# Kernel tuning notes

Hardware: AMD Instinct MI355X
Metric: run time of the kernel (lower is better)

## Reference

```python
import jax, jax.numpy as jnp
import numpy as np

# lower-triangular (row, col) positions in the packed order used by the torch loop:
# index order is (j,i) for j in 0..2, i in 0..j -> (0,0),(1,0),(1,1),(2,0),(2,1),(2,2)
_ROWS = jnp.array([0, 1, 1, 2, 2, 2])
_COLS = jnp.array([0, 0, 1, 0, 1, 2])


def setup_inputs() -> dict:
    key = jax.random.key(0)
    bn, seq_len = 4096, 1024
    chol_cov = jax.random.normal(key, (bn, seq_len, 6), dtype=jnp.float32)
    return {"chol_cov": chol_cov}


def reference(chol_cov) -> jnp.ndarray:
    bn, seq_len, _ = chol_cov.shape
    # scatter packed values into lower-triangular 3x3 L: [bn, seq, 3, 3]
    L = jnp.zeros((bn, seq_len, 3, 3), dtype=chol_cov.dtype)
    L = L.at[..., _ROWS, _COLS].set(chol_cov)
    # Q = L @ L^T, batched tiny 3x3 matmul -> symmetric covariance
    Q = jnp.einsum('bsij,bskj->bsik', L, L)
    return Q
```

## Files before the change

### kernel.cpp

```cpp
#include <hip/hip_runtime.h>


#define THREADS 256
#define ITEMS_PER_BLOCK 1024

__global__ __launch_bounds__(THREADS) void chol_to_cov_kernel(
    const float* __restrict__ in, float* __restrict__ out, long long n_items) {
  __shared__ float s_in[ITEMS_PER_BLOCK * 6];
  __shared__ float s_out[ITEMS_PER_BLOCK * 9];

  const int tid = threadIdx.x;
  const long long block_base = (long long)blockIdx.x * ITEMS_PER_BLOCK;

  if (block_base + ITEMS_PER_BLOCK <= n_items) {
    const float4* __restrict__ in4 = (const float4*)(in + block_base * 6);
    float4* s_in4 = (float4*)s_in;
#pragma unroll
    for (int k = 0; k < 6; k++) {
      s_in4[tid + k * THREADS] = in4[tid + k * THREADS];
    }
    __syncthreads();

#pragma unroll
    for (int k = 0; k < 4; k++) {
      const int item = tid + k * THREADS;
      const float* s = s_in + item * 6;
      const float a = s[0], b = s[1], c = s[2], d = s[3], e = s[4], f = s[5];
      const float q00 = a * a;
      const float q01 = a * b;
      const float q02 = a * d;
      const float q11 = b * b + c * c;
      const float q12 = b * d + c * e;
      const float q22 = d * d + e * e + f * f;
      float* o = s_out + item * 9;
      o[0] = q00;
      o[1] = q01;
      o[2] = q02;
      o[3] = q01;
      o[4] = q11;
      o[5] = q12;
      o[6] = q02;
      o[7] = q12;
      o[8] = q22;
    }
    __syncthreads();

    float4* __restrict__ out4 = (float4*)(out + block_base * 9);
    const float4* s_out4 = (const float4*)s_out;
#pragma unroll
    for (int k = 0; k < 9; k++) {
      out4[tid + k * THREADS] = s_out4[tid + k * THREADS];
    }
  } else {
    for (long long it = block_base + tid; it < n_items; it += THREADS) {
      const float a = in[it * 6 + 0];
      const float b = in[it * 6 + 1];
      const float c = in[it * 6 + 2];
      const float d = in[it * 6 + 3];
      const float e = in[it * 6 + 4];
      const float f = in[it * 6 + 5];
      float* o = out + it * 9;
      o[0] = a * a;
      o[1] = a * b;
      o[2] = a * d;
      o[3] = a * b;
      o[4] = b * b + c * c;
      o[5] = b * d + c * e;
      o[6] = a * d;
      o[7] = b * d + c * e;
      o[8] = d * d + e * e + f * f;
    }
  }
}

extern "C" void kernel_launch(void* const* d_in, const int* in_sizes, int n_in,
                              void* d_out, int out_size, void* d_ws,
                              size_t ws_size, hipStream_t stream) {
  const float* in = (const float*)d_in[0];
  float* out = (float*)d_out;
  const long long n_items = (long long)in_sizes[0] / 6;
  const long long grid =
      (n_items + ITEMS_PER_BLOCK - 1) / ITEMS_PER_BLOCK;
  chol_to_cov_kernel<<<(int)grid, THREADS, 0, stream>>>(in, out, n_items);
}
```

Baseline: 223.6 us.

## Drop shared output staging; compute output float4s directly and use nontemporal loads/stores

Removes the 36KB shared output buffer and its second barrier. Each thread now computes its output float4 straight from the shared input, recomputing the covariance terms for the item that owns it and the next one, then selects the four values with a switch. Global loads and stores use nontemporal builtins to avoid cache pollution on a pure streaming kernel. The lower LDS use should allow more resident blocks, at the cost of redundant arithmetic and a divergent switch per store.

```diff
diff --git a/kernel.cpp b/kernel.cpp
--- a/kernel.cpp
+++ b/kernel.cpp
@@ -2,54 +2,66 @@
 
 
 #define THREADS 256
-#define ITEMS_PER_BLOCK 1024
+#define IPB 1024
+
+typedef float f4 __attribute__((ext_vector_type(4)));
 
 __global__ __launch_bounds__(THREADS) void chol_to_cov_kernel(
     const float* __restrict__ in, float* __restrict__ out, long long n_items) {
-  __shared__ float s_in[ITEMS_PER_BLOCK * 6];
-  __shared__ float s_out[ITEMS_PER_BLOCK * 9];
+  __shared__ float s_in[IPB * 6];
 
   const int tid = threadIdx.x;
-  const long long block_base = (long long)blockIdx.x * ITEMS_PER_BLOCK;
+  const long long block_base = (long long)blockIdx.x * IPB;
 
-  if (block_base + ITEMS_PER_BLOCK <= n_items) {
-    const float4* __restrict__ in4 = (const float4*)(in + block_base * 6);
-    float4* s_in4 = (float4*)s_in;
+  if (block_base + IPB <= n_items) {
+    const f4* __restrict__ in4 = (const f4*)(in + block_base * 6);
+    f4* s4 = (f4*)s_in;
 #pragma unroll
     for (int k = 0; k < 6; k++) {
-      s_in4[tid + k * THREADS] = in4[tid + k * THREADS];
+      const int idx = tid + k * THREADS;
+      s4[idx] = __builtin_nontemporal_load(&in4[idx]);
     }
     __syncthreads();
 
-#pragma unroll
-    for (int k = 0; k < 4; k++) {
-      const int item = tid + k * THREADS;
-      const float* s = s_in + item * 6;
-      const float a = s[0], b = s[1], c = s[2], d = s[3], e = s[4], f = s[5];
-      const float q00 = a * a;
-      const float q01 = a * b;
-      const float q02 = a * d;
-      const float q11 = b * b + c * c;
-      const float q12 = b * d + c * e;
-      const float q22 = d * d + e * e + f * f;
-      float* o = s_out + item * 9;
-      o[0] = q00;
-      o[1] = q01;
-      o[2] = q02;
-      o[3] = q01;
-      o[4] = q11;
-      o[5] = q12;
-      o[6] = q02;
-      o[7] = q12;
-      o[8] = q22;
-    }
-    __syncthreads();
-
-    float4* __restrict__ out4 = (float4*)(out + block_base * 9);
-    const float4* s_out4 = (const float4*)s_out;
+    f4* __restrict__ out4 = (f4*)(out + block_base * 9);
 #pragma unroll
     for (int k = 0; k < 9; k++) {
-      out4[tid + k * THREADS] = s_out4[tid + k * THREADS];
+      const unsigned g = (unsigned)tid + k * THREADS;
+      const unsigned e = 4u * g;
+      const unsigned item = e / 9u;
+      const unsigned r = e - 9u * item;
+      unsigned i1 = item + 1u;
+      if (i1 > IPB - 1u) i1 = IPB - 1u;
+
+      const float* p0 = s_in + item * 6;
+      const float a = p0[0], b = p0[1], c = p0[2];
+      const float d = p0[3], e0 = p0[4], f = p0[5];
+      const float u0 = a * a;
+      const float u1 = a * b;
+      const float u2 = a * d;
+      const float u3 = b * b + c * c;
+      const float u4 = b * d + c * e0;
+      const float u5 = d * d + e0 * e0 + f * f;
+
+      const float* p1 = s_in + i1 * 6;
+      const float a1 = p1[0], b1 = p1[1], d1 = p1[3];
+      const float v0 = a1 * a1;
+      const float v1 = a1 * b1;
+      const float v2 = a1 * d1;
+
+      f4 o;
+      switch (r) {
+        case 0: o = (f4){u0, u1, u2, u1}; break;
+        case 1: o = (f4){u1, u2, u1, u3}; break;
+        case 2: o = (f4){u2, u1, u3, u4}; break;
+        case 3: o = (f4){u1, u3, u4, u2}; break;
+        case 4: o = (f4){u3, u4, u2, u4}; break;
+        case 5: o = (f4){u4, u2, u4, u5}; break;
+        case 6: o = (f4){u2, u4, u5, v0}; break;
+        case 7: o = (f4){u4, u5, v0, v1}; break;
+        default: o = (f4){u5, v0, v1, v2}; break;
+      }
+      __builtin_nontemporal_store(o, &out4[g]);
     }
   } else {
     for (long long it = block_base + tid; it < n_items; it += THREADS) {
@@ -79,7 +91,6 @@
   const float* in = (const float*)d_in[0];
   float* out = (float*)d_out;
   const long long n_items = (long long)in_sizes[0] / 6;
-  const long long grid =
-      (n_items + ITEMS_PER_BLOCK - 1) / ITEMS_PER_BLOCK;
+  const long long grid = (n_items + IPB - 1) / IPB;
   chol_to_cov_kernel<<<(int)grid, THREADS, 0, stream>>>(in, out, n_items);
 }
```

Result: faster. 218.1 us (-2.5%).
